# Kernel tuning notes

Hardware: AMD Instinct MI355X
Metric: run time of the kernel (lower is better)

## Reference

```python
import jax, jax.numpy as jnp
import numpy as np

B, T, C = 4, 2048, 1024
H, E = 4096, 8


def setup_inputs() -> dict:
    key = jax.random.key(0)
    ks = jax.random.split(key, 6)
    scale = 0.02
    x = jax.random.normal(ks[0], (B, T, C), dtype=jnp.float32)
    w_router = jax.random.normal(ks[1], (C, E), dtype=jnp.float32) * scale
    b_router = jnp.zeros((E,), dtype=jnp.float32)
    w1 = jax.random.normal(ks[2], (E, C, H), dtype=jnp.float32) * scale
    b1 = jnp.zeros((E, H), dtype=jnp.float32)
    w2 = jax.random.normal(ks[3], (E, H, C), dtype=jnp.float32) * scale
    b2 = jnp.zeros((E, C), dtype=jnp.float32)
    return {"x": x, "w_router": w_router, "b_router": b_router,
            "w1": w1, "b1": b1, "w2": w2, "b2": b2}


def reference(x, w_router, b_router, w1, b1, w2, b2):
    # Router: logits -> softmax -> top-1 expert index per token
    logits = jnp.einsum('btc,ce->bte', x, w_router) + b_router  # [B,T,E]
    probs = jax.nn.softmax(logits, axis=-1)
    top1 = jnp.argmax(probs, axis=-1)  # [B,T] int

    # Per-expert dense MLP, combined via top-1 mask (masked scatter in torch).
    out = jnp.zeros_like(x)
    for e in range(E):
        h = jax.nn.gelu(jnp.einsum('btc,ch->bth', x, w1[e]) + b1[e],
                        approximate=False)           # [B,T,H]
        y = jnp.einsum('bth,hc->btc', h, w2[e]) + b2[e]  # [B,T,C]
        out = out + jnp.where((top1 == e)[..., None], y, 0.0)
    return out
```

## Files before the change

### kernel.cpp

```cpp
#include <hip/hip_runtime.h>
#include <cstdint>
#include <cstddef>

#define NTOK 8192
#define C_ 1024
#define H_ 4096
#define E_ 8
#define YMAX 72

typedef __attribute__((ext_vector_type(8))) short short8;
typedef __attribute__((ext_vector_type(4))) float f32x4;
typedef __attribute__((ext_vector_type(4))) unsigned int u32x4;

__device__ __forceinline__ uint16_t f2b(float f) {
    uint32_t x;
    __builtin_memcpy(&x, &f, 4);
    x = (x + 0x7fffu + ((x >> 16) & 1u)) >> 16;
    return (uint16_t)x;
}

__device__ __forceinline__ float gelu_f(float v) {
    float u = v * (0.7978845608028654f + 0.03567740814183f * v * v);
    float t = __expf(2.f * u);
    float th = 1.f - 2.f / (t + 1.f);
    return 0.5f * v * (1.f + th);
}

__global__ __launch_bounds__(256) void router_kernel(
    const float* __restrict__ x, const float* __restrict__ wr,
    const float* __restrict__ br, int* __restrict__ top1,
    uint16_t* __restrict__ xb)
{
    int wid = threadIdx.x >> 6, lane = threadIdx.x & 63;
    int tok = blockIdx.x * 4 + wid;
    const float* xrow = x + (size_t)tok * C_;
    uint16_t* xbrow = xb + (size_t)tok * C_;
    float acc[E_];
#pragma unroll
    for (int e = 0; e < E_; e++) acc[e] = 0.f;
#pragma unroll 4
    for (int i = 0; i < C_ / 64; i++) {
        int c = i * 64 + lane;
        float xv = xrow[c];
        xbrow[c] = f2b(xv);
        const f32x4 w0 = *(const f32x4*)(wr + (size_t)c * E_);
        const f32x4 w1v = *(const f32x4*)(wr + (size_t)c * E_ + 4);
#pragma unroll
        for (int e = 0; e < 4; e++) acc[e] += xv * w0[e];
#pragma unroll
        for (int e = 0; e < 4; e++) acc[4 + e] += xv * w1v[e];
    }
#pragma unroll
    for (int off = 32; off > 0; off >>= 1) {
#pragma unroll
        for (int e = 0; e < E_; e++) acc[e] += __shfl_xor(acc[e], off, 64);
    }
    if (lane == 0) {
        float best = acc[0] + br[0];
        int bi = 0;
#pragma unroll
        for (int e = 1; e < E_; e++) {
            float v = acc[e] + br[e];
            if (v > best) { best = v; bi = e; }
        }
        top1[tok] = bi;
    }
}

__global__ void zero_counts(int* counts) {
    if (threadIdx.x < E_) counts[threadIdx.x] = 0;
}

__global__ __launch_bounds__(1024) void scatter_kernel(
    const int* __restrict__ top1, int* counts, int* __restrict__ idx)
{
    __shared__ int lc[E_], base[E_];
    int tid = threadIdx.x;
    if (tid < E_) lc[tid] = 0;
    __syncthreads();
    int t = blockIdx.x * 1024 + tid;
    int e = top1[t];
    int my = atomicAdd(&lc[e], 1);
    __syncthreads();
    if (tid < E_) base[tid] = atomicAdd(&counts[tid], lc[tid]);
    __syncthreads();
    idx[e * NTOK + base[e] + my] = t;
}

__global__ void plan_kernel(const int* __restrict__ counts,
                            int* __restrict__ tab, int* __restrict__ ranges)
{
    if (threadIdx.x == 0) {
        int n = 0, n0 = 0;
        for (int e = 0; e < E_; e++) {
            int nt = (counts[e] + 127) >> 7;
            for (int mb = 0; mb < nt; mb++) tab[n++] = (e << 16) | mb;
            if (e == 3) n0 = n;
        }
        ranges[0] = 0;  ranges[1] = n;
        ranges[2] = 0;  ranges[3] = n0;
        ranges[4] = n0; ranges[5] = n;
    }
}

__global__ __launch_bounds__(256) void transpose_cvt_kernel(
    const float* __restrict__ w, uint16_t* __restrict__ wt,
    int K, int N, int ebase)
{
    __shared__ uint16_t tile[64][66];
    int ez = blockIdx.z, e = ebase + ez;
    int n0 = blockIdx.x * 64, k0 = blockIdx.y * 64;
    int t = threadIdx.x;
#pragma unroll
    for (int i = 0; i < 4; i++) {
        int chunk = i * 256 + t;
        int r = chunk >> 4, c4 = chunk & 15;
        f32x4 v = *(const f32x4*)(w + (size_t)(e * K + k0 + r) * N + n0 + c4 * 4);
        uint32_t u0 = (uint32_t)f2b(v.x) | ((uint32_t)f2b(v.y) << 16);
        uint32_t u1 = (uint32_t)f2b(v.z) | ((uint32_t)f2b(v.w) << 16);
        *(uint32_t*)&tile[r][c4 * 4 + 0] = u0;
        *(uint32_t*)&tile[r][c4 * 4 + 2] = u1;
    }
    __syncthreads();
#pragma unroll
    for (int i = 0; i < 2; i++) {
        int chunk = i * 256 + t;
        int rn = chunk >> 3, ck = chunk & 7;
        uint32_t p[4];
#pragma unroll
        for (int j = 0; j < 4; j++) {
            uint32_t lo = tile[ck * 8 + 2 * j][rn];
            uint32_t hi = tile[ck * 8 + 2 * j + 1][rn];
            p[j] = lo | (hi << 16);
        }
        u32x4 v; v.x = p[0]; v.y = p[1]; v.z = p[2]; v.w = p[3];
        *(u32x4*)(wt + ((size_t)ez * N + n0 + rn) * K + k0 + ck * 8) = v;
    }
}

template <int YB, int K, int N, typename OutT, bool GELU>
__global__ __launch_bounds__(256, 3) void gemm_kernel(
    const uint16_t* __restrict__ A, const uint16_t* __restrict__ Bt,
    const float* __restrict__ bias, OutT* __restrict__ Out,
    const int* __restrict__ counts, const int* __restrict__ idx,
    const int* __restrict__ tab, const int* __restrict__ range, int ebase)
{
    constexpr int BM = 128, BN = 128, NW = 256;
    constexpr int MR = 4;
    constexpr int NITER = K / 32;
    constexpr int GX = N / BN;
    constexpr int NWG = GX * YB;
    static_assert(NWG % 8 == 0, "grid must be divisible by 8 XCDs");
    static_assert((NITER & 1) == 0, "NITER must be even");

    int o = blockIdx.x * YB + blockIdx.y;
    int lid = (o & 7) * (NWG / 8) + (o >> 3);
    int nb = lid / YB;
    int tile = range[0] + lid % YB;
    if (tile >= range[1]) return;
    int ent = tab[tile];
    int e = ent >> 16, mb = ent & 0xffff;
    int ez = e - ebase;
    int cnt = counts[e];

    __shared__ __align__(16) uint16_t As[2][BM][32];
    __shared__ __align__(16) uint16_t Bs[2][BN][32];

    int t = threadIdx.x;
    int lane = t & 63, w = t >> 6;
    int wm = w >> 1, wn = w & 1;

    const int* idxe = idx + e * NTOK;

    f32x4 acc[MR][4];
#pragma unroll
    for (int mt = 0; mt < MR; mt++)
#pragma unroll
        for (int nt = 0; nt < 4; nt++) acc[mt][nt] = (f32x4)(0.f);

    const uint16_t* Bte = Bt + ((size_t)ez * N + (size_t)nb * BN) * K;

    const uint16_t* aptr[2];
    const uint16_t* bptr[2];
#pragma unroll
    for (int i = 0; i < 2; i++) {
        int cid = i * NW + t;
        int r = cid >> 2, j = cid & 3;
        int s = mb * BM + r;
        int tk = idxe[(s < cnt) ? s : 0];
        aptr[i] = A + (size_t)tk * K + (j ^ ((r >> 1) & 3)) * 8;
    }
#pragma unroll
    for (int i = 0; i < 2; i++) {
        int cid = i * NW + t;
        int r = cid >> 2, j = cid & 3;
        bptr[i] = Bte + (size_t)r * K + (j ^ ((r >> 1) & 3)) * 8;
    }

    u32x4 ra[2], rb[2];
    auto loadreg = [&](int kt) {
        int k0 = kt * 32;
#pragma unroll
        for (int i = 0; i < 2; i++) ra[i] = *(const u32x4*)(aptr[i] + k0);
#pragma unroll
        for (int i = 0; i < 2; i++) rb[i] = *(const u32x4*)(bptr[i] + k0);
    };
    auto ldswrite = [&](int sel) {
#pragma unroll
        for (int i = 0; i < 2; i++)
            *(u32x4*)(&As[sel][0][0] + (size_t)(i * NW + t) * 8) = ra[i];
#pragma unroll
        for (int i = 0; i < 2; i++)
            *(u32x4*)(&Bs[sel][0][0] + (size_t)(i * NW + t) * 8) = rb[i];
    };

    int cs = (((lane >> 4) ^ ((lane & 15) >> 1)) & 3) * 8;

    auto compute = [&](int sel) {
        short8 af[MR], bf[4];
#pragma unroll
        for (int mt = 0; mt < MR; mt++)
            af[mt] = *(const short8*)
                (&As[sel][0][0] + (wm * 64 + mt * 16 + (lane & 15)) * 32 + cs);
#pragma unroll
        for (int nt = 0; nt < 4; nt++)
            bf[nt] = *(const short8*)
                (&Bs[sel][0][0] + (wn * 64 + nt * 16 + (lane & 15)) * 32 + cs);
#pragma unroll
        for (int mt = 0; mt < MR; mt++)
#pragma unroll
            for (int nt = 0; nt < 4; nt++)
                acc[mt][nt] = __builtin_amdgcn_mfma_f32_16x16x32_bf16(
                    af[mt], bf[nt], acc[mt][nt], 0, 0, 0);
    };

    loadreg(0);
    ldswrite(0);
    __syncthreads();

    for (int kt = 0; kt + 2 < NITER; kt += 2) {
        loadreg(kt + 1);
        __builtin_amdgcn_sched_barrier(0);
        compute(0);
        ldswrite(1);
        __syncthreads();
        loadreg(kt + 2);
        __builtin_amdgcn_sched_barrier(0);
        compute(1);
        ldswrite(0);
        __syncthreads();
    }
    loadreg(NITER - 1);
    __builtin_amdgcn_sched_barrier(0);
    compute(0);
    ldswrite(1);
    __syncthreads();
    compute(1);

    const float* be = bias + (size_t)e * N;
#pragma unroll
    for (int mt = 0; mt < MR; mt++) {
        int rbase = wm * 64 + mt * 16 + (lane >> 4) * 4;
#pragma unroll
        for (int r = 0; r < 4; r++) {
            int row = rbase + r;
            int s = mb * BM + row;
            if (s < cnt) {
                int tk = idxe[s];
#pragma unroll
                for (int nt = 0; nt < 4; nt++) {
                    int gcol = nb * BN + wn * 64 + nt * 16 + (lane & 15);
                    float v = acc[mt][nt][r] + be[gcol];
                    if (GELU) v = gelu_f(v);
                    if constexpr (sizeof(OutT) == 2)
                        Out[(size_t)tk * N + gcol] = (OutT)f2b(v);
                    else
                        Out[(size_t)tk * N + gcol] = v;
                }
            }
        }
    }
}

extern "C" void kernel_launch(void* const* d_in, const int* in_sizes, int n_in,
                              void* d_out, int out_size, void* d_ws, size_t ws_size,
                              hipStream_t stream)
{
    const float* x  = (const float*)d_in[0];
    const float* wr = (const float*)d_in[1];
    const float* br = (const float*)d_in[2];
    const float* b1 = (const float*)d_in[4];
    const float* w1 = (const float*)d_in[3];
    const float* w2 = (const float*)d_in[5];
    const float* b2 = (const float*)d_in[6];
    float* out = (float*)d_out;

    char* ws = (char*)d_ws;
    int* counts    = (int*)ws;
    int* top1      = (int*)(ws + 1024);
    int* idx       = (int*)(ws + 64 * 1024);
    int* tab       = (int*)(ws + 392 * 1024);
    int* ranges    = (int*)(ws + 396 * 1024);
    uint16_t* xb   = (uint16_t*)(ws + ((size_t)1 << 20));
    uint16_t* hbuf = (uint16_t*)(ws + ((size_t)17 << 20));
    uint16_t* wT   = (uint16_t*)(ws + ((size_t)81 << 20));

    bool big = ws_size >= ((size_t)145 << 20);

    hipLaunchKernelGGL(zero_counts, dim3(1), dim3(64), 0, stream, counts);
    hipLaunchKernelGGL(router_kernel, dim3(NTOK / 4), dim3(256), 0, stream,
                       x, wr, br, top1, xb);
    hipLaunchKernelGGL(scatter_kernel, dim3(NTOK / 1024), dim3(1024), 0, stream,
                       top1, counts, idx);
    hipLaunchKernelGGL(plan_kernel, dim3(1), dim3(64), 0, stream,
                       counts, tab, ranges);

    if (big) {
        hipLaunchKernelGGL(transpose_cvt_kernel, dim3(H_ / 64, C_ / 64, E_),
                           dim3(256), 0, stream, w1, wT, C_, H_, 0);
        hipLaunchKernelGGL((gemm_kernel<YMAX, C_, H_, uint16_t, true>),
                           dim3(H_ / 128, YMAX, 1), dim3(256), 0, stream,
                           xb, wT, b1, hbuf, counts, idx, tab, ranges, 0);
        hipLaunchKernelGGL(transpose_cvt_kernel, dim3(C_ / 64, H_ / 64, E_),
                           dim3(256), 0, stream, w2, wT, H_, C_, 0);
        hipLaunchKernelGGL((gemm_kernel<YMAX, H_, C_, float, false>),
                           dim3(C_ / 128, YMAX, 1), dim3(256), 0, stream,
                           hbuf, wT, b2, out, counts, idx, tab, ranges, 0);
    } else {
        for (int c = 0; c < 2; c++) {
            hipLaunchKernelGGL(transpose_cvt_kernel, dim3(H_ / 64, C_ / 64, 4),
                               dim3(256), 0, stream, w1, wT, C_, H_, c * 4);
            hipLaunchKernelGGL((gemm_kernel<YMAX, C_, H_, uint16_t, true>),
                               dim3(H_ / 128, YMAX, 1), dim3(256), 0, stream,
                               xb, wT, b1, hbuf, counts, idx, tab, ranges + 2 + 2 * c, c * 4);
        }
        for (int c = 0; c < 2; c++) {
            hipLaunchKernelGGL(transpose_cvt_kernel, dim3(C_ / 64, H_ / 64, 4),
                               dim3(256), 0, stream, w2, wT, H_, C_, c * 4);
            hipLaunchKernelGGL((gemm_kernel<YMAX, H_, C_, float, false>),
                               dim3(C_ / 128, YMAX, 1), dim3(256), 0, stream,
                               hbuf, wT, b2, out, counts, idx, tab, ranges + 2 + 2 * c, c * 4);
        }
    }
}
```

Baseline: 568.2 us.

## Fuse weight transposes into router and GEMM launches, drop plan kernel

The w1 transpose-convert now runs as extra blocks of the router kernel, and the w2 transpose runs as extra blocks of the first GEMM launch, so weight preparation shares launches with compute. The zero_counts and plan kernels are gone: counts are zeroed in the router and each GEMM block derives its expert and M-tile from counts directly. The GEMM main loop is restructured to use two register buffers with explicit lgkmcnt waits and barriers, aiming for deeper global-load prefetch. This needs a larger workspace to hold both transposed weight buffers, and the fused transpose blocks compete with GEMM blocks for compute units.

New measurement: 573.4 us. About the same (+0.9%).

```diff
diff --git a/kernel.cpp b/kernel.cpp
--- a/kernel.cpp
+++ b/kernel.cpp
@@ -7,6 +7,9 @@
 #define H_ 4096
 #define E_ 8
 #define YMAX 72
+#define RB_ (NTOK / 4)
+#define TB1_ ((H_ / 64) * (C_ / 64) * E_)
+#define TB2_ ((C_ / 64) * (H_ / 64) * E_)
 
 typedef __attribute__((ext_vector_type(8))) short short8;
 typedef __attribute__((ext_vector_type(4))) float f32x4;
@@ -26,13 +29,73 @@
     return 0.5f * v * (1.f + th);
 }
 
-__global__ __launch_bounds__(256) void router_kernel(
+#define BAR_LGKM() do {                                             \
+    __builtin_amdgcn_sched_barrier(0);                              \
+    asm volatile("s_waitcnt lgkmcnt(0)" ::: "memory");              \
+    __builtin_amdgcn_sched_barrier(0);                              \
+    __builtin_amdgcn_s_barrier();                                   \
+    __builtin_amdgcn_sched_barrier(0);                              \
+} while (0)
+
+__device__ __forceinline__ void transpose_tile_body(
+    const float* __restrict__ w, uint16_t* __restrict__ wt,
+    int K, int N, int e, int ez, int n0, int k0, uint16_t (*tile)[66])
+{
+    int t = threadIdx.x;
+#pragma unroll
+    for (int i = 0; i < 4; i++) {
+        int chunk = i * 256 + t;
+        int r = chunk >> 4, c4 = chunk & 15;
+        f32x4 v = *(const f32x4*)(w + (size_t)(e * K + k0 + r) * N + n0 + c4 * 4);
+        uint32_t u0 = (uint32_t)f2b(v.x) | ((uint32_t)f2b(v.y) << 16);
+        uint32_t u1 = (uint32_t)f2b(v.z) | ((uint32_t)f2b(v.w) << 16);
+        *(uint32_t*)&tile[r][c4 * 4 + 0] = u0;
+        *(uint32_t*)&tile[r][c4 * 4 + 2] = u1;
+    }
+    __syncthreads();
+#pragma unroll
+    for (int i = 0; i < 2; i++) {
+        int chunk = i * 256 + t;
+        int rn = chunk >> 3, ck = chunk & 7;
+        uint32_t p[4];
+#pragma unroll
+        for (int j = 0; j < 4; j++) {
+            uint32_t lo = tile[ck * 8 + 2 * j][rn];
+            uint32_t hi = tile[ck * 8 + 2 * j + 1][rn];
+            p[j] = lo | (hi << 16);
+        }
+        u32x4 v; v.x = p[0]; v.y = p[1]; v.z = p[2]; v.w = p[3];
+        *(u32x4*)(wt + ((size_t)ez * N + n0 + rn) * K + k0 + ck * 8) = v;
+    }
+}
+
+__global__ __launch_bounds__(256) void transpose_cvt_kernel(
+    const float* __restrict__ w, uint16_t* __restrict__ wt,
+    int K, int N, int ebase)
+{
+    __shared__ uint16_t tile[64][66];
+    int ez = blockIdx.z;
+    transpose_tile_body(w, wt, K, N, ebase + ez, ez,
+                        blockIdx.x * 64, blockIdx.y * 64, tile);
+}
+
+__global__ __launch_bounds__(256) void router_t1_kernel(
     const float* __restrict__ x, const float* __restrict__ wr,
     const float* __restrict__ br, int* __restrict__ top1,
-    uint16_t* __restrict__ xb)
-{
+    uint16_t* __restrict__ xb, int* __restrict__ counts,
+    const float* __restrict__ w1, uint16_t* __restrict__ wt1)
+{
+    __shared__ uint16_t tile[64][66];
+    int bid = blockIdx.x;
+    if (bid >= RB_) {
+        int b = bid - RB_;
+        int xq = b & 63, yq = (b >> 6) & 15, z = b >> 10;
+        transpose_tile_body(w1, wt1, C_, H_, z, z, xq * 64, yq * 64, tile);
+        return;
+    }
+    if (bid == 0 && threadIdx.x < E_) counts[threadIdx.x] = 0;
     int wid = threadIdx.x >> 6, lane = threadIdx.x & 63;
-    int tok = blockIdx.x * 4 + wid;
+    int tok = bid * 4 + wid;
     const float* xrow = x + (size_t)tok * C_;
     uint16_t* xbrow = xb + (size_t)tok * C_;
     float acc[E_];
@@ -65,10 +128,6 @@
         }
         top1[tok] = bi;
     }
-}
-
-__global__ void zero_counts(int* counts) {
-    if (threadIdx.x < E_) counts[threadIdx.x] = 0;
 }
 
 __global__ __launch_bounds__(1024) void scatter_kernel(
@@ -87,84 +146,58 @@
     idx[e * NTOK + base[e] + my] = t;
 }
 
-__global__ void plan_kernel(const int* __restrict__ counts,
-                            int* __restrict__ tab, int* __restrict__ ranges)
-{
-    if (threadIdx.x == 0) {
-        int n = 0, n0 = 0;
-        for (int e = 0; e < E_; e++) {
-            int nt = (counts[e] + 127) >> 7;
-            for (int mb = 0; mb < nt; mb++) tab[n++] = (e << 16) | mb;
-            if (e == 3) n0 = n;
-        }
-        ranges[0] = 0;  ranges[1] = n;
-        ranges[2] = 0;  ranges[3] = n0;
-        ranges[4] = n0; ranges[5] = n;
-    }
-}
-
-__global__ __launch_bounds__(256) void transpose_cvt_kernel(
-    const float* __restrict__ w, uint16_t* __restrict__ wt,
-    int K, int N, int ebase)
-{
-    __shared__ uint16_t tile[64][66];
-    int ez = blockIdx.z, e = ebase + ez;
-    int n0 = blockIdx.x * 64, k0 = blockIdx.y * 64;
-    int t = threadIdx.x;
-#pragma unroll
-    for (int i = 0; i < 4; i++) {
-        int chunk = i * 256 + t;
-        int r = chunk >> 4, c4 = chunk & 15;
-        f32x4 v = *(const f32x4*)(w + (size_t)(e * K + k0 + r) * N + n0 + c4 * 4);
-        uint32_t u0 = (uint32_t)f2b(v.x) | ((uint32_t)f2b(v.y) << 16);
-        uint32_t u1 = (uint32_t)f2b(v.z) | ((uint32_t)f2b(v.w) << 16);
-        *(uint32_t*)&tile[r][c4 * 4 + 0] = u0;
-        *(uint32_t*)&tile[r][c4 * 4 + 2] = u1;
-    }
-    __syncthreads();
-#pragma unroll
-    for (int i = 0; i < 2; i++) {
-        int chunk = i * 256 + t;
-        int rn = chunk >> 3, ck = chunk & 7;
-        uint32_t p[4];
-#pragma unroll
-        for (int j = 0; j < 4; j++) {
-            uint32_t lo = tile[ck * 8 + 2 * j][rn];
-            uint32_t hi = tile[ck * 8 + 2 * j + 1][rn];
-            p[j] = lo | (hi << 16);
-        }
-        u32x4 v; v.x = p[0]; v.y = p[1]; v.z = p[2]; v.w = p[3];
-        *(u32x4*)(wt + ((size_t)ez * N + n0 + rn) * K + k0 + ck * 8) = v;
-    }
-}
-
-template <int YB, int K, int N, typename OutT, bool GELU>
+template <int GX, int YB, int K, int N, typename OutT, bool GELU,
+          int TB, int TNX, int TKY, int TK, int TN>
 __global__ __launch_bounds__(256, 3) void gemm_kernel(
     const uint16_t* __restrict__ A, const uint16_t* __restrict__ Bt,
     const float* __restrict__ bias, OutT* __restrict__ Out,
     const int* __restrict__ counts, const int* __restrict__ idx,
-    const int* __restrict__ tab, const int* __restrict__ range, int ebase)
+    int e0, int ne, const float* __restrict__ wsrc, uint16_t* __restrict__ wdst)
 {
     constexpr int BM = 128, BN = 128, NW = 256;
     constexpr int MR = 4;
     constexpr int NITER = K / 32;
-    constexpr int GX = N / BN;
     constexpr int NWG = GX * YB;
     static_assert(NWG % 8 == 0, "grid must be divisible by 8 XCDs");
-    static_assert((NITER & 1) == 0, "NITER must be even");
-
-    int o = blockIdx.x * YB + blockIdx.y;
+    static_assert(NITER >= 4 && (NITER & 1) == 0, "NITER even >= 4");
+
+    __shared__ __align__(16) uint16_t As[2][BM][32];
+    __shared__ __align__(16) uint16_t Bs[2][BN][32];
+    __shared__ uint16_t tile[TB > 0 ? 64 : 1][66];
+
+    int bid = blockIdx.x;
+    if constexpr (TB > 0) {
+        if (bid >= NWG) {
+            int b = bid - NWG;
+            int xq = b % TNX, yq = (b / TNX) % TKY, z = b / (TNX * TKY);
+            transpose_tile_body(wsrc, wdst, TK, TN, z, z, xq * 64, yq * 64, tile);
+            return;
+        }
+    }
+
+    int o = bid;
     int lid = (o & 7) * (NWG / 8) + (o >> 3);
     int nb = lid / YB;
-    int tile = range[0] + lid % YB;
-    if (tile >= range[1]) return;
-    int ent = tab[tile];
-    int e = ent >> 16, mb = ent & 0xffff;
-    int ez = e - ebase;
-    int cnt = counts[e];
-
-    __shared__ __align__(16) uint16_t As[2][BM][32];
-    __shared__ __align__(16) uint16_t Bs[2][BN][32];
+    int tl = lid % YB;
+
+    int cn[E_];
+    {
+        const int4 c0 = *(const int4*)counts;
+        const int4 c1 = *(const int4*)(counts + 4);
+        cn[0] = c0.x; cn[1] = c0.y; cn[2] = c0.z; cn[3] = c0.w;
+        cn[4] = c1.x; cn[5] = c1.y; cn[6] = c1.z; cn[7] = c1.w;
+    }
+    int e = -1, mb = 0, cnt = 0;
+#pragma unroll
+    for (int q = 0; q < E_; ++q) {
+        if (q >= e0 && q < e0 + ne && e < 0) {
+            int nt = (cn[q] + 127) >> 7;
+            if (tl < nt) { e = q; mb = tl; cnt = cn[q]; }
+            else tl -= nt;
+        }
+    }
+    if (e < 0) return;
+    int ez = e - e0;
 
     int t = threadIdx.x;
     int lane = t & 63, w = t >> 6;
@@ -197,21 +230,32 @@
         bptr[i] = Bte + (size_t)r * K + (j ^ ((r >> 1) & 3)) * 8;
     }
 
-    u32x4 ra[2], rb[2];
-    auto loadreg = [&](int kt) {
+    u32x4 ra0[2], rb0[2], ra1[2], rb1[2];
+    auto loadA = [&](int kt) {
         int k0 = kt * 32;
-#pragma unroll
-        for (int i = 0; i < 2; i++) ra[i] = *(const u32x4*)(aptr[i] + k0);
-#pragma unroll
-        for (int i = 0; i < 2; i++) rb[i] = *(const u32x4*)(bptr[i] + k0);
+        ra0[0] = *(const u32x4*)(aptr[0] + k0);
+        ra0[1] = *(const u32x4*)(aptr[1] + k0);
+        rb0[0] = *(const u32x4*)(bptr[0] + k0);
+        rb0[1] = *(const u32x4*)(bptr[1] + k0);
     };
-    auto ldswrite = [&](int sel) {
-#pragma unroll
-        for (int i = 0; i < 2; i++)
-            *(u32x4*)(&As[sel][0][0] + (size_t)(i * NW + t) * 8) = ra[i];
-#pragma unroll
-        for (int i = 0; i < 2; i++)
-            *(u32x4*)(&Bs[sel][0][0] + (size_t)(i * NW + t) * 8) = rb[i];
+    auto loadB = [&](int kt) {
+        int k0 = kt * 32;
+        ra1[0] = *(const u32x4*)(aptr[0] + k0);
+        ra1[1] = *(const u32x4*)(aptr[1] + k0);
+        rb1[0] = *(const u32x4*)(bptr[0] + k0);
+        rb1[1] = *(const u32x4*)(bptr[1] + k0);
+    };
+    auto writeA = [&]() {
+        *(u32x4*)(&As[0][0][0] + (size_t)t * 8) = ra0[0];
+        *(u32x4*)(&As[0][0][0] + (size_t)(NW + t) * 8) = ra0[1];
+        *(u32x4*)(&Bs[0][0][0] + (size_t)t * 8) = rb0[0];
+        *(u32x4*)(&Bs[0][0][0] + (size_t)(NW + t) * 8) = rb0[1];
+    };
+    auto writeB = [&]() {
+        *(u32x4*)(&As[1][0][0] + (size_t)t * 8) = ra1[0];
+        *(u32x4*)(&As[1][0][0] + (size_t)(NW + t) * 8) = ra1[1];
+        *(u32x4*)(&Bs[1][0][0] + (size_t)t * 8) = rb1[0];
+        *(u32x4*)(&Bs[1][0][0] + (size_t)(NW + t) * 8) = rb1[1];
     };
 
     int cs = (((lane >> 4) ^ ((lane & 15) >> 1)) & 3) * 8;
@@ -234,27 +278,30 @@
                     af[mt], bf[nt], acc[mt][nt], 0, 0, 0);
     };
 
-    loadreg(0);
-    ldswrite(0);
-    __syncthreads();
-
-    for (int kt = 0; kt + 2 < NITER; kt += 2) {
-        loadreg(kt + 1);
+    loadA(0);
+    loadB(1);
+    writeA();
+    BAR_LGKM();
+
+    int kt = 0;
+    for (; kt + 3 < NITER; kt += 2) {
+        loadA(kt + 2);
         __builtin_amdgcn_sched_barrier(0);
         compute(0);
-        ldswrite(1);
-        __syncthreads();
-        loadreg(kt + 2);
+        __builtin_amdgcn_sched_barrier(0);
+        writeB();
+        BAR_LGKM();
+        loadB(kt + 3);
         __builtin_amdgcn_sched_barrier(0);
         compute(1);
-        ldswrite(0);
-        __syncthreads();
-    }
-    loadreg(NITER - 1);
+        __builtin_amdgcn_sched_barrier(0);
+        writeA();
+        BAR_LGKM();
+    }
+    compute(0);
     __builtin_amdgcn_sched_barrier(0);
-    compute(0);
-    ldswrite(1);
-    __syncthreads();
+    writeB();
+    BAR_LGKM();
     compute(1);
 
     const float* be = bias + (size_t)e * N;
@@ -299,47 +346,67 @@
     int* counts    = (int*)ws;
     int* top1      = (int*)(ws + 1024);
     int* idx       = (int*)(ws + 64 * 1024);
-    int* tab       = (int*)(ws + 392 * 1024);
-    int* ranges    = (int*)(ws + 396 * 1024);
     uint16_t* xb   = (uint16_t*)(ws + ((size_t)1 << 20));
     uint16_t* hbuf = (uint16_t*)(ws + ((size_t)17 << 20));
-    uint16_t* wT   = (uint16_t*)(ws + ((size_t)81 << 20));
-
-    bool big = ws_size >= ((size_t)145 << 20);
-
-    hipLaunchKernelGGL(zero_counts, dim3(1), dim3(64), 0, stream, counts);
-    hipLaunchKernelGGL(router_kernel, dim3(NTOK / 4), dim3(256), 0, stream,
-                       x, wr, br, top1, xb);
-    hipLaunchKernelGGL(scatter_kernel, dim3(NTOK / 1024), dim3(1024), 0, stream,
-                       top1, counts, idx);
-    hipLaunchKernelGGL(plan_kernel, dim3(1), dim3(64), 0, stream,
-                       counts, tab, ranges);
-
-    if (big) {
-        hipLaunchKernelGGL(transpose_cvt_kernel, dim3(H_ / 64, C_ / 64, E_),
-                           dim3(256), 0, stream, w1, wT, C_, H_, 0);
-        hipLaunchKernelGGL((gemm_kernel<YMAX, C_, H_, uint16_t, true>),
-                           dim3(H_ / 128, YMAX, 1), dim3(256), 0, stream,
-                           xb, wT, b1, hbuf, counts, idx, tab, ranges, 0);
+    uint16_t* wT1  = (uint16_t*)(ws + ((size_t)81 << 20));
+    uint16_t* wT2  = (uint16_t*)(ws + ((size_t)145 << 20));
+
+    bool t1 = ws_size >= ((size_t)209 << 20);
+    bool t2 = ws_size >= ((size_t)145 << 20);
+
+    if (t1) {
+        hipLaunchKernelGGL(router_t1_kernel, dim3(RB_ + TB1_), dim3(256), 0,
+                           stream, x, wr, br, top1, xb, counts, w1, wT1);
+        hipLaunchKernelGGL(scatter_kernel, dim3(NTOK / 1024), dim3(1024), 0,
+                           stream, top1, counts, idx);
+        hipLaunchKernelGGL((gemm_kernel<H_ / 128, YMAX, C_, H_, uint16_t, true,
+                                        TB2_, C_ / 64, H_ / 64, H_, C_>),
+                           dim3(H_ / 128 * YMAX + TB2_), dim3(256), 0, stream,
+                           xb, wT1, b1, hbuf, counts, idx, 0, E_, w2, wT2);
+        hipLaunchKernelGGL((gemm_kernel<C_ / 128, YMAX, H_, C_, float, false,
+                                        0, 1, 1, 1, 1>),
+                           dim3(C_ / 128 * YMAX), dim3(256), 0, stream,
+                           hbuf, wT2, b2, out, counts, idx, 0, E_,
+                           (const float*)nullptr, (uint16_t*)nullptr);
+    } else if (t2) {
+        hipLaunchKernelGGL(router_t1_kernel, dim3(RB_ + TB1_), dim3(256), 0,
+                           stream, x, wr, br, top1, xb, counts, w1, wT1);
+        hipLaunchKernelGGL(scatter_kernel, dim3(NTOK / 1024), dim3(1024), 0,
+                           stream, top1, counts, idx);
+        hipLaunchKernelGGL((gemm_kernel<H_ / 128, YMAX, C_, H_, uint16_t, true,
+                                        0, 1, 1, 1, 1>),
+                           dim3(H_ / 128 * YMAX), dim3(256), 0, stream,
+                           xb, wT1, b1, hbuf, counts, idx, 0, E_,
+                           (const float*)nullptr, (uint16_t*)nullptr);
         hipLaunchKernelGGL(transpose_cvt_kernel, dim3(C_ / 64, H_ / 64, E_),
-                           dim3(256), 0, stream, w2, wT, H_, C_, 0);
-        hipLaunchKernelGGL((gemm_kernel<YMAX, H_, C_, float, false>),
-                           dim3(C_ / 128, YMAX, 1), dim3(256), 0, stream,
-                           hbuf, wT, b2, out, counts, idx, tab, ranges, 0);
+                           dim3(256), 0, stream, w2, wT1, H_, C_, 0);
+        hipLaunchKernelGGL((gemm_kernel<C_ / 128, YMAX, H_, C_, float, false,
+                                        0, 1, 1, 1, 1>),
+                           dim3(C_ / 128 * YMAX), dim3(256), 0, stream,
+                           hbuf, wT1, b2, out, counts, idx, 0, E_,
+                           (const float*)nullptr, (uint16_t*)nullptr);
     } else {
+        hipLaunchKernelGGL(router_t1_kernel, dim3(RB_), dim3(256), 0,
+                           stream, x, wr, br, top1, xb, counts, w1, wT1);
+        hipLaunchKernelGGL(scatter_kernel, dim3(NTOK / 1024), dim3(1024), 0,
+                           stream, top1, counts, idx);
         for (int c = 0; c < 2; c++) {
             hipLaunchKernelGGL(transpose_cvt_kernel, dim3(H_ / 64, C_ / 64, 4),
-                               dim3(256), 0, stream, w1, wT, C_, H_, c * 4);
-            hipLaunchKernelGGL((gemm_kernel<YMAX, C_, H_, uint16_t, true>),
-                               dim3(H_ / 128, YMAX, 1), dim3(256), 0, stream,
-                               xb, wT, b1, hbuf, counts, idx, tab, ranges + 2 + 2 * c, c * 4);
+                               dim3(256), 0, stream, w1, wT1, C_, H_, c * 4);
+            hipLaunchKernelGGL((gemm_kernel<H_ / 128, YMAX, C_, H_, uint16_t, true,
+                                            0, 1, 1, 1, 1>),
+                               dim3(H_ / 128 * YMAX), dim3(256), 0, stream,
+                               xb, wT1, b1, hbuf, counts, idx, c * 4, 4,
+                               (const float*)nullptr, (uint16_t*)nullptr);
         }
         for (int c = 0; c < 2; c++) {
             hipLaunchKernelGGL(transpose_cvt_kernel, dim3(C_ / 64, H_ / 64, 4),
-                               dim3(256), 0, stream, w2, wT, H_, C_, c * 4);
-            hipLaunchKernelGGL((gemm_kernel<YMAX, H_, C_, float, false>),
-                               dim3(C_ / 128, YMAX, 1), dim3(256), 0, stream,
-                               hbuf, wT, b2, out, counts, idx, tab, ranges + 2 + 2 * c, c * 4);
-        }
-    }
-}
+                               dim3(256), 0, stream, w2, wT1, H_, C_, c * 4);
+            hipLaunchKernelGGL((gemm_kernel<C_ / 128, YMAX, H_, C_, float, false,
+                                            0, 1, 1, 1, 1>),
+                               dim3(C_ / 128 * YMAX), dim3(256), 0, stream,
+                               hbuf, wT1, b2, out, counts, idx, c * 4, 4,
+                               (const float*)nullptr, (uint16_t*)nullptr);
+        }
+    }
+}
```
